# Performance work log

Measured on AMD Instinct MI355X. Metric: run time of the kernel, lower is better.

The kernel has to match this reference:

```python
import jax, jax.numpy as jnp
import numpy as np

B, H, N, L = 8, 128, 64, 8192
LOG_DT_MIN, LOG_DT_MAX = float(np.log(0.001)), float(np.log(0.1))


def setup_inputs() -> dict:
    key = jax.random.key(0)
    k_x, k_are, k_aim, k_c, k_dt = jax.random.split(key, 5)
    x = jax.random.normal(k_x, (B, H, L), dtype=jnp.float32)
    # A_re: negative real parts (clipped to <= -1e-4 in forward anyway)
    A_re = -jax.random.uniform(k_are, (H, N, 1), dtype=jnp.float32, minval=0.1, maxval=1.0)
    A_im = jax.random.normal(k_aim, (H, N, 1), dtype=jnp.float32) * float(np.pi)
    C = (0.5 ** 0.5) * jax.random.normal(k_c, (H, N, 2), dtype=jnp.float32)
    D = jnp.ones((1, H, 1), dtype=jnp.float32)
    u = jax.random.uniform(k_dt, (H, 1, 1), dtype=jnp.float32)
    log_delta = u * (LOG_DT_MAX - LOG_DT_MIN) + LOG_DT_MIN
    return {"x": x, "A_re": A_re, "A_im": A_im, "C": C, "D": D, "log_delta": log_delta}


def reference(x, A_re, A_im, C, D, log_delta):
    seq_len = x.shape[-1]
    # ---- S4D-ZOH kernel generation ----
    A = jnp.minimum(A_re, -1e-4) + 1j * A_im            # (H, N, 1) complex
    Cc = C[..., 0:1] + 1j * C[..., 1:2]                 # (H, N, 1) complex
    step = jnp.exp(log_delta)                           # (H, 1, 1)
    dA = step * A                                       # (H, N, 1)
    times = jnp.arange(seq_len, dtype=jnp.float32)[None, None, :]  # (1, 1, L)
    part = jnp.exp(times * dA)                          # (H, N, L)
    cons = (jnp.exp(dA) - 1.0) / A                      # (H, N, 1)
    K = jnp.sum(Cc * cons * part, axis=-2).real         # (H, L)
    # ---- causal conv via FFT (torch pads both to length 2L) ----
    n = seq_len + K.shape[-1]                           # 2L
    xd = jnp.fft.rfft(x, n=n, axis=-1)                  # (B, H, L+1)
    Kd = jnp.fft.rfft(K[None], n=n, axis=-1)            # (1, H, L+1)
    conv = jnp.fft.irfft(xd * Kd, n=n, axis=-1)[:, :, :seq_len]
    return conv + D * x
```

## Files before the change

### kernel.cpp

```cpp
#include <hip/hip_runtime.h>
#include <hip/hip_bf16.h>
#include <math.h>

#define B_ 8
#define H_ 128
#define N_ 64
#define L_ 8192
#define MCH 64
#define SCH (L_ / MCH)
#define EROW 136

#define LDS_TBL   34816
#define LDS_SEG   51200
#define LDS_KV    53248
#define LDS_TOTAL 53504

typedef __attribute__((ext_vector_type(8))) short bf16x8;
typedef __attribute__((ext_vector_type(4))) float f32x4;

__device__ __forceinline__ float bf2f(ushort s) { return __uint_as_float(((uint)s) << 16); }
__device__ __forceinline__ uint packbf2(float a, float b) {
    __hip_bfloat162 h = __float22bfloat162_rn(make_float2(a, b));
    union { __hip_bfloat162 h2; uint u; } cv; cv.h2 = h;
    return cv.u;
}
__device__ __forceinline__ bf16x8 pack_bf8(f32x4 a, f32x4 b) {
    union { uint u[4]; bf16x8 v; } r;
    r.u[0] = packbf2(a[0], a[1]); r.u[1] = packbf2(a[2], a[3]);
    r.u[2] = packbf2(b[0], b[1]); r.u[3] = packbf2(b[2], b[3]);
    return r.v;
}

__global__ __launch_bounds__(256, 3) void s4d_fused(
    const float* __restrict__ x,
    const float* __restrict__ A_re, const float* __restrict__ A_im,
    const float* __restrict__ Cp, const float* __restrict__ Dp,
    const float* __restrict__ log_delta,
    float* __restrict__ out)
{
    __shared__ __align__(16) char lds[LDS_TOTAL];
    ushort* EBUF  = (ushort*)lds;
    char*   TBLb  = lds + LDS_TBL;
    float*  segr  = (float*)(lds + LDS_SEG);
    float*  segi  = segr + 256;
    float*  kv    = (float*)(lds + LDS_KV);

    const int seq = blockIdx.x;
    const int h   = seq % H_;
    const int tid = threadIdx.x;
    const int w   = tid >> 6;
    const int lane = tid & 63;
    const int n16 = lane & 15, q = lane >> 4;
    const int n = lane;
    const int g = w;

    float are = fminf(A_re[h * N_ + n], -1e-4f);
    float aim = A_im[h * N_ + n];
    float step = expf(log_delta[h]);
    float dre = step * are, dim = step * aim;
    float er = expf(dre);
    float sd, cd; sincosf(dim, &sd, &cd);
    float rre = er * cd, rim = er * sd;
    float cre = Cp[(h * N_ + n) * 2 + 0];
    float cim = Cp[(h * N_ + n) * 2 + 1];
    float inv  = 1.0f / (are * are + aim * aim);
    float numr = rre - 1.0f, numi = rim;
    float consr = (numr * are + numi * aim) * inv;
    float consi = (numi * are - numr * aim) * inv;
    float wr = cre * consr - cim * consi;
    float wi = cre * consi + cim * consr;
    float dval = Dp[h];
    float m64r = rre, m64i = rim;
#pragma unroll
    for (int k = 0; k < 6; ++k) { float tr = m64r*m64r - m64i*m64i, ti = 2.f*m64r*m64i; m64r = tr; m64i = ti; }

    auto rp = [&](float d, float& pr, float& pi) {
        float ex = __expf(d * dre);
        float ang = d * dim;
        float s = __sinf(ang), c2 = __cosf(ang);
        pr = ex * c2; pi = ex * s;
    };

    const float* xs = x + (size_t)seq * L_;
    bf16x8 xbv[2][2];
#pragma unroll
    for (int ic = 0; ic < 2; ++ic) {
        int c = (2 * w + ic) * 16 + n16;
#pragma unroll
        for (int kc = 0; kc < 2; ++kc) {
            const float* p = xs + c * MCH + kc * 32 + q * 8;
            f32x4 f0 = __builtin_nontemporal_load((const f32x4*)p);
            f32x4 f1 = __builtin_nontemporal_load((const f32x4*)p + 1);
            xbv[ic][kc] = pack_bf8(f0, f1);
        }
    }

    {
        uint qr[8], qi[8];
#pragma unroll
        for (int i = 0; i < 8; ++i) {
            int t0 = g * 16 + 2 * i;
            float ar0, ai0, ar1, ai1;
            rp((float)(63 - t0), ar0, ai0);
            rp((float)(62 - t0), ar1, ai1);
            qr[i] = packbf2(ar0, ar1);
            qi[i] = packbf2(ai0, ai1);
        }
        const int ra = 2 * n, rb = 2 * n + 1;
        const uint xa = (uint)(ra & 7) << 4, xbm = (uint)(rb & 7) << 4;
        *(uint4*)(TBLb + ((ra * 128 + g * 32     ) ^ xa)) = ((uint4*)qr)[0];
        *(uint4*)(TBLb + ((ra * 128 + g * 32 + 16) ^ xa)) = ((uint4*)qr)[1];
        *(uint4*)(TBLb + ((rb * 128 + g * 32     ) ^ xbm)) = ((uint4*)qi)[0];
        *(uint4*)(TBLb + ((rb * 128 + g * 32 + 16) ^ xbm)) = ((uint4*)qi)[1];
    }

    {
        float kvloc[16];
#pragma unroll
        for (int j = 0; j < 16; ++j) {
            float pr, pi; rp((float)(g * 16 + j), pr, pi);
            kvloc[j] = wr * pr - wi * pi;
        }
#pragma unroll
        for (int j = 0; j < 16; ++j) {
#pragma unroll
            for (int s = 1; s < 64; s <<= 1)
                kvloc[j] += __shfl_xor(kvloc[j], s, 64);
        }
#pragma unroll
        for (int j = 0; j < 16; ++j)
            if (n == j) kv[g * 16 + j] = kvloc[j];
    }
    __syncthreads();

    const uint xr = (uint)(n16 & 7) << 4;
#pragma unroll
    for (int rt = 0; rt < 8; ++rt) {
        int row = rt * 16 + n16;
        bf16x8 a0 = *(const bf16x8*)(TBLb + ((row * 128      + q * 16) ^ xr));
        bf16x8 a1 = *(const bf16x8*)(TBLb + ((row * 128 + 64 + q * 16) ^ xr));
#pragma unroll
        for (int ic = 0; ic < 2; ++ic) {
            f32x4 acc = {0.f, 0.f, 0.f, 0.f};
            acc = __builtin_amdgcn_mfma_f32_16x16x32_bf16(a0, xbv[ic][0], acc, 0, 0, 0);
            acc = __builtin_amdgcn_mfma_f32_16x16x32_bf16(a1, xbv[ic][1], acc, 0, 0, 0);
            int c = (2 * w + ic) * 16 + n16;
            uint2 st = make_uint2(packbf2(acc[0], acc[1]), packbf2(acc[2], acc[3]));
            *(uint2*)&EBUF[c * EROW + rt * 16 + q * 4] = st;
        }
    }

    float mr = m64r, mi = m64i;
    float m32r = mr, m32i = mi;
#pragma unroll
    for (int k = 0; k < 5; ++k) {
        float tr = m32r * m32r - m32i * m32i, ti = 2.f * m32r * m32i;
        m32r = tr; m32i = ti;
    }

    {
        float sr = 0.f, si = 0.f;
#pragma unroll
        for (int j = 0; j < 32; ++j) {
            uint e = *(const uint*)&EBUF[(g * 32 + j) * EROW + 2 * n];
            float er2 = bf2f((ushort)(e & 0xffffu)), ei2 = bf2f((ushort)(e >> 16));
            float nr = er2 + mr * sr - mi * si;
            float ni = ei2 + mr * si + mi * sr;
            sr = nr; si = ni;
        }
        segr[g * 64 + n] = sr; segi[g * 64 + n] = si;
    }

    f32x4 accT[4][2];
#pragma unroll
    for (int rt = 0; rt < 4; ++rt) {
        int row = rt * 16 + n16;
        union { uint u[4]; bf16x8 v; } f0, f1;
#pragma unroll
        for (int kc = 0; kc < 2; ++kc) {
#pragma unroll
            for (int ki = 0; ki < 4; ++ki) {
                int t0 = kc * 32 + q * 8 + 2 * ki;
                int i0 = row - t0, i1 = i0 - 1;
                float v0 = kv[i0 & 63]; v0 = (i0 >= 0) ? v0 : 0.f; if (i0 == 0) v0 += dval;
                float v1 = kv[i1 & 63]; v1 = (i1 >= 0) ? v1 : 0.f; if (i1 == 0) v1 += dval;
                if (kc == 0) f0.u[ki] = packbf2(v0, v1); else f1.u[ki] = packbf2(v0, v1);
            }
        }
#pragma unroll
        for (int ic = 0; ic < 2; ++ic) {
            f32x4 a = {0.f, 0.f, 0.f, 0.f};
            a = __builtin_amdgcn_mfma_f32_16x16x32_bf16(f0.v, xbv[ic][0], a, 0, 0, 0);
            a = __builtin_amdgcn_mfma_f32_16x16x32_bf16(f1.v, xbv[ic][1], a, 0, 0, 0);
            accT[rt][ic] = a;
        }
    }
    __syncthreads();

#pragma unroll
    for (int i = 0; i < 16; ++i) {
        int j = g * 16 + i;
        float pr, pi; rp((float)(j + 1), pr, pi);
        float ur = wr * pr - wi * pi;
        float ui = wr * pi + wi * pr;
        *(uint*)(TBLb + ((j * 256 + n * 4) ^ ((uint)(j & 7) << 4))) = packbf2(ur, -ui);
    }

    {
        float pr2 = 0.f, pi2 = 0.f;
        for (int gp = 0; gp < g; ++gp) {
            float Er = segr[gp * 64 + n], Ei = segi[gp * 64 + n];
            float nr = Er + m32r * pr2 - m32i * pi2;
            float ni = Ei + m32r * pi2 + m32i * pr2;
            pr2 = nr; pi2 = ni;
        }
        float sr = pr2, si = pi2;
#pragma unroll
        for (int j = 0; j < 32; ++j) {
            uint* ep = (uint*)&EBUF[(g * 32 + j) * EROW + 2 * n];
            uint e = *ep;
            float er2 = bf2f((ushort)(e & 0xffffu)), ei2 = bf2f((ushort)(e >> 16));
            *ep = packbf2(sr, si);
            float nr = er2 + mr * sr - mi * si;
            float ni = ei2 + mr * si + mi * sr;
            sr = nr; si = ni;
        }
    }
    __syncthreads();

    float* op = out + (size_t)seq * L_;
#pragma unroll
    for (int rt = 0; rt < 4; ++rt) {
        int row = rt * 16 + n16;
        bf16x8 p0 = *(const bf16x8*)(TBLb + ((row * 256       + q * 16) ^ xr));
        bf16x8 p1 = *(const bf16x8*)(TBLb + ((row * 256 +  64 + q * 16) ^ xr));
        bf16x8 p2 = *(const bf16x8*)(TBLb + ((row * 256 + 128 + q * 16) ^ xr));
        bf16x8 p3 = *(const bf16x8*)(TBLb + ((row * 256 + 192 + q * 16) ^ xr));
#pragma unroll
        for (int ic = 0; ic < 2; ++ic) {
            int c = (2 * w + ic) * 16 + n16;
            f32x4 accP = {0.f, 0.f, 0.f, 0.f};
            accP = __builtin_amdgcn_mfma_f32_16x16x32_bf16(p0,
                       *(const bf16x8*)&EBUF[c * EROW +       q * 8], accP, 0, 0, 0);
            accP = __builtin_amdgcn_mfma_f32_16x16x32_bf16(p1,
                       *(const bf16x8*)&EBUF[c * EROW +  32 + q * 8], accP, 0, 0, 0);
            accP = __builtin_amdgcn_mfma_f32_16x16x32_bf16(p2,
                       *(const bf16x8*)&EBUF[c * EROW +  64 + q * 8], accP, 0, 0, 0);
            accP = __builtin_amdgcn_mfma_f32_16x16x32_bf16(p3,
                       *(const bf16x8*)&EBUF[c * EROW +  96 + q * 8], accP, 0, 0, 0);
            f32x4 o;
            o[0] = accT[rt][ic][0] + accP[0];
            o[1] = accT[rt][ic][1] + accP[1];
            o[2] = accT[rt][ic][2] + accP[2];
            o[3] = accT[rt][ic][3] + accP[3];
            __builtin_nontemporal_store(o, (f32x4*)(op + c * MCH + rt * 16 + q * 4));
        }
    }
}

extern "C" void kernel_launch(void* const* d_in, const int* in_sizes, int n_in,
                              void* d_out, int out_size, void* d_ws, size_t ws_size,
                              hipStream_t stream)
{
    const float* x  = (const float*)d_in[0];
    const float* Ar = (const float*)d_in[1];
    const float* Ai = (const float*)d_in[2];
    const float* C  = (const float*)d_in[3];
    const float* D  = (const float*)d_in[4];
    const float* ld = (const float*)d_in[5];
    float* out = (float*)d_out;
    (void)d_ws; (void)ws_size;

    hipLaunchKernelGGL(s4d_fused, dim3(B_ * H_), dim3(256), 0, stream,
                       x, Ar, Ai, C, D, ld, out);
}
```

Measured before the change: 109.0 us.

## Process two batch sequences per block to amortize per-head table generation

Each block now handles two batch elements that share the same head h, so the SSM coefficients, the Q and P projection tables, the kv kernel taps and the Toeplitz fragments are built once and reused for both sequences. The P table gets its own LDS region instead of overwriting the Q table, and the second sequence's input is loaded early as raw fp32 and packed to bf16 later. The grid is halved and launch bounds drop to 2 blocks per CU to fit the larger LDS footprint. This trades lower occupancy and higher register pressure from the extra prefetched data for less redundant transcendental and table-building work.

Result: faster. 103.8 us (-4.8%).

```diff
diff --git a/kernel.cpp b/kernel.cpp
--- a/kernel.cpp
+++ b/kernel.cpp
@@ -9,11 +9,13 @@
 #define MCH 64
 #define SCH (L_ / MCH)
 #define EROW 136
-
-#define LDS_TBL   34816
-#define LDS_SEG   51200
-#define LDS_KV    53248
-#define LDS_TOTAL 53504
+#define NSEQ 2
+
+#define LDS_Q     34816
+#define LDS_P     51200
+#define LDS_SEG   67584
+#define LDS_KV    71680
+#define LDS_TOTAL 71936
 
 typedef __attribute__((ext_vector_type(8))) short bf16x8;
 typedef __attribute__((ext_vector_type(4))) float f32x4;
@@ -31,7 +33,7 @@
     return r.v;
 }
 
-__global__ __launch_bounds__(256, 3) void s4d_fused(
+__global__ __launch_bounds__(256, 2) void s4d_fused(
     const float* __restrict__ x,
     const float* __restrict__ A_re, const float* __restrict__ A_im,
     const float* __restrict__ Cp, const float* __restrict__ Dp,
@@ -39,20 +41,19 @@
     float* __restrict__ out)
 {
     __shared__ __align__(16) char lds[LDS_TOTAL];
-    ushort* EBUF  = (ushort*)lds;
-    char*   TBLb  = lds + LDS_TBL;
-    float*  segr  = (float*)(lds + LDS_SEG);
-    float*  segi  = segr + 256;
-    float*  kv    = (float*)(lds + LDS_KV);
-
-    const int seq = blockIdx.x;
-    const int h   = seq % H_;
+    ushort* EBUF = (ushort*)lds;
+    char*   QTBL = lds + LDS_Q;
+    char*   PTBL = lds + LDS_P;
+    float*  seg  = (float*)(lds + LDS_SEG);
+    float*  kv   = (float*)(lds + LDS_KV);
+
+    const int h   = blockIdx.x % H_;
+    const int bp  = blockIdx.x / H_;
     const int tid = threadIdx.x;
     const int w   = tid >> 6;
     const int lane = tid & 63;
     const int n16 = lane & 15, q = lane >> 4;
-    const int n = lane;
-    const int g = w;
+    const int n = lane, g = w;
 
     float are = fminf(A_re[h * N_ + n], -1e-4f);
     float aim = A_im[h * N_ + n];
@@ -73,6 +74,10 @@
     float m64r = rre, m64i = rim;
 #pragma unroll
     for (int k = 0; k < 6; ++k) { float tr = m64r*m64r - m64i*m64i, ti = 2.f*m64r*m64i; m64r = tr; m64i = ti; }
+    const float mr = m64r, mi = m64i;
+    float m32r = mr, m32i = mi;
+#pragma unroll
+    for (int k = 0; k < 5; ++k) { float tr = m32r*m32r - m32i*m32i, ti = 2.f*m32r*m32i; m32r = tr; m32i = ti; }
 
     auto rp = [&](float d, float& pr, float& pi) {
         float ex = __expf(d * dre);
@@ -81,17 +86,25 @@
         pr = ex * c2; pi = ex * s;
     };
 
-    const float* xs = x + (size_t)seq * L_;
-    bf16x8 xbv[2][2];
+    const float* xs0 = x   + ((size_t)(2 * bp) * H_ + h) * L_;
+    const float* xs1 = xs0 + (size_t)H_ * L_;
+    float* op0 = out + ((size_t)(2 * bp) * H_ + h) * L_;
+    float* op1 = op0 + (size_t)H_ * L_;
+
+    bf16x8 xb0[2][2];
+    f32x4 raw1[2][2][2];
 #pragma unroll
     for (int ic = 0; ic < 2; ++ic) {
         int c = (2 * w + ic) * 16 + n16;
 #pragma unroll
         for (int kc = 0; kc < 2; ++kc) {
-            const float* p = xs + c * MCH + kc * 32 + q * 8;
-            f32x4 f0 = __builtin_nontemporal_load((const f32x4*)p);
-            f32x4 f1 = __builtin_nontemporal_load((const f32x4*)p + 1);
-            xbv[ic][kc] = pack_bf8(f0, f1);
+            const float* p0 = xs0 + c * MCH + kc * 32 + q * 8;
+            f32x4 f0 = __builtin_nontemporal_load((const f32x4*)p0);
+            f32x4 f1 = __builtin_nontemporal_load((const f32x4*)p0 + 1);
+            xb0[ic][kc] = pack_bf8(f0, f1);
+            const float* p1 = xs1 + c * MCH + kc * 32 + q * 8;
+            raw1[ic][kc][0] = __builtin_nontemporal_load((const f32x4*)p1);
+            raw1[ic][kc][1] = __builtin_nontemporal_load((const f32x4*)p1 + 1);
         }
     }
 
@@ -108,10 +121,10 @@
         }
         const int ra = 2 * n, rb = 2 * n + 1;
         const uint xa = (uint)(ra & 7) << 4, xbm = (uint)(rb & 7) << 4;
-        *(uint4*)(TBLb + ((ra * 128 + g * 32     ) ^ xa)) = ((uint4*)qr)[0];
-        *(uint4*)(TBLb + ((ra * 128 + g * 32 + 16) ^ xa)) = ((uint4*)qr)[1];
-        *(uint4*)(TBLb + ((rb * 128 + g * 32     ) ^ xbm)) = ((uint4*)qi)[0];
-        *(uint4*)(TBLb + ((rb * 128 + g * 32 + 16) ^ xbm)) = ((uint4*)qi)[1];
+        *(uint4*)(QTBL + ((ra * 128 + g * 32     ) ^ xa))  = ((uint4*)qr)[0];
+        *(uint4*)(QTBL + ((ra * 128 + g * 32 + 16) ^ xa))  = ((uint4*)qr)[1];
+        *(uint4*)(QTBL + ((rb * 128 + g * 32     ) ^ xbm)) = ((uint4*)qi)[0];
+        *(uint4*)(QTBL + ((rb * 128 + g * 32 + 16) ^ xbm)) = ((uint4*)qi)[1];
     }
 
     {
@@ -131,47 +144,18 @@
         for (int j = 0; j < 16; ++j)
             if (n == j) kv[g * 16 + j] = kvloc[j];
     }
+
+#pragma unroll
+    for (int i = 0; i < 16; ++i) {
+        int j = g * 16 + i;
+        float pr, pi; rp((float)(j + 1), pr, pi);
+        float ur = wr * pr - wi * pi;
+        float ui = wr * pi + wi * pr;
+        *(uint*)(PTBL + ((j * 256 + n * 4) ^ ((uint)(j & 7) << 4))) = packbf2(ur, -ui);
+    }
     __syncthreads();
 
-    const uint xr = (uint)(n16 & 7) << 4;
-#pragma unroll
-    for (int rt = 0; rt < 8; ++rt) {
-        int row = rt * 16 + n16;
-        bf16x8 a0 = *(const bf16x8*)(TBLb + ((row * 128      + q * 16) ^ xr));
-        bf16x8 a1 = *(const bf16x8*)(TBLb + ((row * 128 + 64 + q * 16) ^ xr));
-#pragma unroll
-        for (int ic = 0; ic < 2; ++ic) {
-            f32x4 acc = {0.f, 0.f, 0.f, 0.f};
-            acc = __builtin_amdgcn_mfma_f32_16x16x32_bf16(a0, xbv[ic][0], acc, 0, 0, 0);
-            acc = __builtin_amdgcn_mfma_f32_16x16x32_bf16(a1, xbv[ic][1], acc, 0, 0, 0);
-            int c = (2 * w + ic) * 16 + n16;
-            uint2 st = make_uint2(packbf2(acc[0], acc[1]), packbf2(acc[2], acc[3]));
-            *(uint2*)&EBUF[c * EROW + rt * 16 + q * 4] = st;
-        }
-    }
-
-    float mr = m64r, mi = m64i;
-    float m32r = mr, m32i = mi;
-#pragma unroll
-    for (int k = 0; k < 5; ++k) {
-        float tr = m32r * m32r - m32i * m32i, ti = 2.f * m32r * m32i;
-        m32r = tr; m32i = ti;
-    }
-
-    {
-        float sr = 0.f, si = 0.f;
-#pragma unroll
-        for (int j = 0; j < 32; ++j) {
-            uint e = *(const uint*)&EBUF[(g * 32 + j) * EROW + 2 * n];
-            float er2 = bf2f((ushort)(e & 0xffffu)), ei2 = bf2f((ushort)(e >> 16));
-            float nr = er2 + mr * sr - mi * si;
-            float ni = ei2 + mr * si + mi * sr;
-            sr = nr; si = ni;
-        }
-        segr[g * 64 + n] = sr; segi[g * 64 + n] = si;
-    }
-
-    f32x4 accT[4][2];
+    bf16x8 tf[4][2];
 #pragma unroll
     for (int rt = 0; rt < 4; ++rt) {
         int row = rt * 16 + n16;
@@ -187,75 +171,116 @@
                 if (kc == 0) f0.u[ki] = packbf2(v0, v1); else f1.u[ki] = packbf2(v0, v1);
             }
         }
-#pragma unroll
-        for (int ic = 0; ic < 2; ++ic) {
-            f32x4 a = {0.f, 0.f, 0.f, 0.f};
-            a = __builtin_amdgcn_mfma_f32_16x16x32_bf16(f0.v, xbv[ic][0], a, 0, 0, 0);
-            a = __builtin_amdgcn_mfma_f32_16x16x32_bf16(f1.v, xbv[ic][1], a, 0, 0, 0);
-            accT[rt][ic] = a;
-        }
-    }
-    __syncthreads();
-
-#pragma unroll
-    for (int i = 0; i < 16; ++i) {
-        int j = g * 16 + i;
-        float pr, pi; rp((float)(j + 1), pr, pi);
-        float ur = wr * pr - wi * pi;
-        float ui = wr * pi + wi * pr;
-        *(uint*)(TBLb + ((j * 256 + n * 4) ^ ((uint)(j & 7) << 4))) = packbf2(ur, -ui);
-    }
-
-    {
-        float pr2 = 0.f, pi2 = 0.f;
-        for (int gp = 0; gp < g; ++gp) {
-            float Er = segr[gp * 64 + n], Ei = segi[gp * 64 + n];
-            float nr = Er + m32r * pr2 - m32i * pi2;
-            float ni = Ei + m32r * pi2 + m32i * pr2;
-            pr2 = nr; pi2 = ni;
-        }
-        float sr = pr2, si = pi2;
-#pragma unroll
-        for (int j = 0; j < 32; ++j) {
-            uint* ep = (uint*)&EBUF[(g * 32 + j) * EROW + 2 * n];
-            uint e = *ep;
-            float er2 = bf2f((ushort)(e & 0xffffu)), ei2 = bf2f((ushort)(e >> 16));
-            *ep = packbf2(sr, si);
-            float nr = er2 + mr * sr - mi * si;
-            float ni = ei2 + mr * si + mi * sr;
-            sr = nr; si = ni;
-        }
-    }
-    __syncthreads();
-
-    float* op = out + (size_t)seq * L_;
-#pragma unroll
-    for (int rt = 0; rt < 4; ++rt) {
-        int row = rt * 16 + n16;
-        bf16x8 p0 = *(const bf16x8*)(TBLb + ((row * 256       + q * 16) ^ xr));
-        bf16x8 p1 = *(const bf16x8*)(TBLb + ((row * 256 +  64 + q * 16) ^ xr));
-        bf16x8 p2 = *(const bf16x8*)(TBLb + ((row * 256 + 128 + q * 16) ^ xr));
-        bf16x8 p3 = *(const bf16x8*)(TBLb + ((row * 256 + 192 + q * 16) ^ xr));
-#pragma unroll
-        for (int ic = 0; ic < 2; ++ic) {
-            int c = (2 * w + ic) * 16 + n16;
-            f32x4 accP = {0.f, 0.f, 0.f, 0.f};
-            accP = __builtin_amdgcn_mfma_f32_16x16x32_bf16(p0,
-                       *(const bf16x8*)&EBUF[c * EROW +       q * 8], accP, 0, 0, 0);
-            accP = __builtin_amdgcn_mfma_f32_16x16x32_bf16(p1,
-                       *(const bf16x8*)&EBUF[c * EROW +  32 + q * 8], accP, 0, 0, 0);
-            accP = __builtin_amdgcn_mfma_f32_16x16x32_bf16(p2,
-                       *(const bf16x8*)&EBUF[c * EROW +  64 + q * 8], accP, 0, 0, 0);
-            accP = __builtin_amdgcn_mfma_f32_16x16x32_bf16(p3,
-                       *(const bf16x8*)&EBUF[c * EROW +  96 + q * 8], accP, 0, 0, 0);
-            f32x4 o;
-            o[0] = accT[rt][ic][0] + accP[0];
-            o[1] = accT[rt][ic][1] + accP[1];
-            o[2] = accT[rt][ic][2] + accP[2];
-            o[3] = accT[rt][ic][3] + accP[3];
-            __builtin_nontemporal_store(o, (f32x4*)(op + c * MCH + rt * 16 + q * 4));
-        }
-    }
+        tf[rt][0] = f0.v; tf[rt][1] = f1.v;
+    }
+
+    const uint xr = (uint)(n16 & 7) << 4;
+
+    auto do_seq = [&](const bf16x8 (&xb)[2][2], int sb, float* op) {
+#pragma unroll
+        for (int rt = 0; rt < 8; ++rt) {
+            int row = rt * 16 + n16;
+            bf16x8 a0 = *(const bf16x8*)(QTBL + ((row * 128      + q * 16) ^ xr));
+            bf16x8 a1 = *(const bf16x8*)(QTBL + ((row * 128 + 64 + q * 16) ^ xr));
+#pragma unroll
+            for (int ic = 0; ic < 2; ++ic) {
+                f32x4 acc = {0.f, 0.f, 0.f, 0.f};
+                acc = __builtin_amdgcn_mfma_f32_16x16x32_bf16(a0, xb[ic][0], acc, 0, 0, 0);
+                acc = __builtin_amdgcn_mfma_f32_16x16x32_bf16(a1, xb[ic][1], acc, 0, 0, 0);
+                int c = (2 * w + ic) * 16 + n16;
+                uint2 st = make_uint2(packbf2(acc[0], acc[1]), packbf2(acc[2], acc[3]));
+                *(uint2*)&EBUF[c * EROW + rt * 16 + q * 4] = st;
+            }
+        }
+
+        float* sr_ = seg + sb * 512;
+        float* si_ = sr_ + 256;
+        {
+            float sr = 0.f, si = 0.f;
+#pragma unroll
+            for (int j = 0; j < 32; ++j) {
+                uint e = *(const uint*)&EBUF[(g * 32 + j) * EROW + 2 * n];
+                float er2 = bf2f((ushort)(e & 0xffffu)), ei2 = bf2f((ushort)(e >> 16));
+                float nr = er2 + mr * sr - mi * si;
+                float ni = ei2 + mr * si + mi * sr;
+                sr = nr; si = ni;
+            }
+            sr_[g * 64 + n] = sr; si_[g * 64 + n] = si;
+        }
+
+        f32x4 accT[4][2];
+#pragma unroll
+        for (int rt = 0; rt < 4; ++rt) {
+#pragma unroll
+            for (int ic = 0; ic < 2; ++ic) {
+                f32x4 a = {0.f, 0.f, 0.f, 0.f};
+                a = __builtin_amdgcn_mfma_f32_16x16x32_bf16(tf[rt][0], xb[ic][0], a, 0, 0, 0);
+                a = __builtin_amdgcn_mfma_f32_16x16x32_bf16(tf[rt][1], xb[ic][1], a, 0, 0, 0);
+                accT[rt][ic] = a;
+            }
+        }
+        __syncthreads();
+
+        {
+            float pr2 = 0.f, pi2 = 0.f;
+            for (int gp = 0; gp < g; ++gp) {
+                float Er = sr_[gp * 64 + n], Ei = si_[gp * 64 + n];
+                float nr = Er + m32r * pr2 - m32i * pi2;
+                float ni = Ei + m32r * pi2 + m32i * pr2;
+                pr2 = nr; pi2 = ni;
+            }
+            float sr = pr2, si = pi2;
+#pragma unroll
+            for (int j = 0; j < 32; ++j) {
+                uint* ep = (uint*)&EBUF[(g * 32 + j) * EROW + 2 * n];
+                uint e = *ep;
+                float er2 = bf2f((ushort)(e & 0xffffu)), ei2 = bf2f((ushort)(e >> 16));
+                *ep = packbf2(sr, si);
+                float nr = er2 + mr * sr - mi * si;
+                float ni = ei2 + mr * si + mi * sr;
+                sr = nr; si = ni;
+            }
+        }
+
+#pragma unroll
+        for (int rt = 0; rt < 4; ++rt) {
+            int row = rt * 16 + n16;
+            bf16x8 p0 = *(const bf16x8*)(PTBL + ((row * 256       + q * 16) ^ xr));
+            bf16x8 p1 = *(const bf16x8*)(PTBL + ((row * 256 +  64 + q * 16) ^ xr));
+            bf16x8 p2 = *(const bf16x8*)(PTBL + ((row * 256 + 128 + q * 16) ^ xr));
+            bf16x8 p3 = *(const bf16x8*)(PTBL + ((row * 256 + 192 + q * 16) ^ xr));
+#pragma unroll
+            for (int ic = 0; ic < 2; ++ic) {
+                int c = (2 * w + ic) * 16 + n16;
+                f32x4 accP = {0.f, 0.f, 0.f, 0.f};
+                accP = __builtin_amdgcn_mfma_f32_16x16x32_bf16(p0,
+                           *(const bf16x8*)&EBUF[c * EROW +       q * 8], accP, 0, 0, 0);
+                accP = __builtin_amdgcn_mfma_f32_16x16x32_bf16(p1,
+                           *(const bf16x8*)&EBUF[c * EROW +  32 + q * 8], accP, 0, 0, 0);
+                accP = __builtin_amdgcn_mfma_f32_16x16x32_bf16(p2,
+                           *(const bf16x8*)&EBUF[c * EROW +  64 + q * 8], accP, 0, 0, 0);
+                accP = __builtin_amdgcn_mfma_f32_16x16x32_bf16(p3,
+                           *(const bf16x8*)&EBUF[c * EROW +  96 + q * 8], accP, 0, 0, 0);
+                f32x4 o;
+                o[0] = accT[rt][ic][0] + accP[0];
+                o[1] = accT[rt][ic][1] + accP[1];
+                o[2] = accT[rt][ic][2] + accP[2];
+                o[3] = accT[rt][ic][3] + accP[3];
+                __builtin_nontemporal_store(o, (f32x4*)(op + c * MCH + rt * 16 + q * 4));
+            }
+        }
+    };
+
+    do_seq(xb0, 0, op0);
+
+    bf16x8 xb1[2][2];
+#pragma unroll
+    for (int ic = 0; ic < 2; ++ic)
+#pragma unroll
+        for (int kc = 0; kc < 2; ++kc)
+            xb1[ic][kc] = pack_bf8(raw1[ic][kc][0], raw1[ic][kc][1]);
+
+    do_seq(xb1, 1, op1);
 }
 
 extern "C" void kernel_launch(void* const* d_in, const int* in_sizes, int n_in,
@@ -271,6 +296,6 @@
     float* out = (float*)d_out;
     (void)d_ws; (void)ws_size;
 
-    hipLaunchKernelGGL(s4d_fused, dim3(B_ * H_), dim3(256), 0, stream,
+    hipLaunchKernelGGL(s4d_fused, dim3(B_ * H_ / NSEQ), dim3(256), 0, stream,
                        x, Ar, Ai, C, D, ld, out);
 }
```
